# Optimization experiments

Hardware: AMD Instinct MI355X
Metric: run time of the kernel (lower is better)

The kernel has to match this reference:

```python
import jax, jax.numpy as jnp
import numpy as np

B, S, D, H = 2, 2048, 2048, 16
DH = D // H  # 128
ROPE_BASE = 10000.0


def setup_inputs() -> dict:
    key = jax.random.key(0)
    ks = jax.random.split(key, 5)
    scale = 0.02
    return {
        "x": jax.random.normal(ks[0], (B, S, D), dtype=jnp.float32),
        "wq": jax.random.normal(ks[1], (D, D), dtype=jnp.float32) * scale,
        "wk": jax.random.normal(ks[2], (D, D), dtype=jnp.float32) * scale,
        "wv": jax.random.normal(ks[3], (D, D), dtype=jnp.float32) * scale,
        "wo": jax.random.normal(ks[4], (D, D), dtype=jnp.float32) * scale,
    }


def _rope_cache(seq_len, dhead):
    # flash-attn RotaryEmbedding: inv_freq over even dims, full rotary_dim = dhead
    inv_freq = 1.0 / (ROPE_BASE ** (jnp.arange(0, dhead, 2, dtype=jnp.float32) / dhead))
    t = jnp.arange(seq_len, dtype=jnp.float32)
    freqs = jnp.einsum("s,d->sd", t, inv_freq)  # [S, DH/2]
    return jnp.cos(freqs), jnp.sin(freqs)


def _apply_rope_interleaved(t, cos, sin):
    # t: [B, S, H, DH]; interleaved pairs (t[...,0::2], t[...,1::2])
    te, to = t[..., 0::2], t[..., 1::2]
    c = cos[None, :, None, :]
    s = sin[None, :, None, :]
    re = te * c - to * s
    ro = te * s + to * c
    return jnp.stack([re, ro], axis=-1).reshape(t.shape)


def reference(x, wq, wk, wv, wo):
    b, s, d = x.shape
    q = (x @ wq).reshape(b, s, H, DH)
    k = (x @ wk).reshape(b, s, H, DH)
    v = (x @ wv).reshape(b, s, H, DH)

    cos, sin = _rope_cache(s, DH)
    q = _apply_rope_interleaved(q.astype(jnp.float32), cos, sin)
    k = _apply_rope_interleaved(k.astype(jnp.float32), cos, sin)

    # flash_attn_func(causal=True) semantics: bf16 inputs, fp32 softmax, scale 1/sqrt(dhead)
    qb = q.astype(jnp.bfloat16)
    kb = k.astype(jnp.bfloat16)
    vb = v.astype(jnp.bfloat16)
    scale = 1.0 / np.sqrt(DH)
    scores = jnp.einsum("bqhd,bkhd->bhqk", qb, kb,
                        preferred_element_type=jnp.float32) * scale
    causal = jnp.tril(jnp.ones((s, s), dtype=bool))
    scores = jnp.where(causal[None, None], scores, -jnp.inf)
    p = jax.nn.softmax(scores, axis=-1)  # fp32
    attn = jnp.einsum("bhqk,bkhd->bqhd", p.astype(jnp.bfloat16), vb,
                      preferred_element_type=jnp.float32)
    attn = attn.astype(jnp.bfloat16).astype(x.dtype)  # flash returns bf16, then .to(x)
    out = attn.reshape(b, s, d) @ wo
    return out
```

## Files before the change

kernel.cpp:

```cpp
#include <hip/hip_runtime.h>
#include <hip/hip_bf16.h>
#include <stdint.h>

#define B_SZ   2
#define S_LEN  2048
#define DMODEL 2048
#define NH     16
#define DHD    128

typedef __attribute__((ext_vector_type(8))) __bf16 bf16x8;
typedef __attribute__((ext_vector_type(4))) float  f32x4;
typedef __attribute__((ext_vector_type(4))) float  float4v;
typedef __attribute__((ext_vector_type(8))) unsigned short ushort8;
typedef __attribute__((ext_vector_type(4))) unsigned short ushort4v;

__device__ __forceinline__ unsigned short f2bf(float f) {
  unsigned int u = __float_as_uint(f);
  unsigned int r = (u + 0x7fffu + ((u >> 16) & 1u)) >> 16;
  return (unsigned short)r;
}

__device__ __forceinline__ unsigned int cvt_pk_bf16(float lo, float hi) {
  unsigned int r;
  asm("v_cvt_pk_bf16_f32 %0, %1, %2" : "=v"(r) : "v"(lo), "v"(hi));
  return r;
}

__device__ __forceinline__ void async_cp16(void* lds, const void* g) {
  __builtin_amdgcn_global_load_lds(
      (const __attribute__((address_space(1))) void*)g,
      (__attribute__((address_space(3))) void*)lds, 16, 0, 0);
}

__global__ __launch_bounds__(256) void k_cast_bf16(const float* __restrict__ in,
                                                   unsigned short* __restrict__ out,
                                                   int n4) {
  int i = blockIdx.x * 256 + threadIdx.x;
  if (i >= n4) return;
  float4v v = ((const float4v*)in)[i];
  ushort4v o;
  o[0] = f2bf(v[0]); o[1] = f2bf(v[1]); o[2] = f2bf(v[2]); o[3] = f2bf(v[3]);
  ((ushort4v*)out)[i] = o;
}

__global__ __launch_bounds__(256) void k_transpose_all(const float* __restrict__ w0,
                                                       const float* __restrict__ w1,
                                                       const float* __restrict__ w2,
                                                       const float* __restrict__ w3,
                                                       unsigned short* __restrict__ WTbase) {
  __shared__ unsigned short tile[64 * 72];
  const int z = blockIdx.z;
  const float* W = (z == 0) ? w0 : (z == 1) ? w1 : (z == 2) ? w2 : w3;
  unsigned short* WT = WTbase + (size_t)z * 4194304;
  const int n0 = blockIdx.x * 64;
  const int k0 = blockIdx.y * 64;
  const int t = threadIdx.x;
#pragma unroll
  for (int i = 0; i < 4; ++i) {
    int c = t + 256 * i;
    int r = c >> 4, c4 = c & 15;
    float4v v = *(const float4v*)(W + (size_t)(k0 + r) * DMODEL + n0 + c4 * 4);
    ushort4v o;
    o[0] = f2bf(v[0]); o[1] = f2bf(v[1]); o[2] = f2bf(v[2]); o[3] = f2bf(v[3]);
    *(ushort4v*)(&tile[r * 72 + c4 * 4]) = o;
  }
  __syncthreads();
#pragma unroll
  for (int i = 0; i < 2; ++i) {
    int c = t + 256 * i;
    int n = c >> 3, k8 = c & 7;
    ushort8 o;
#pragma unroll
    for (int j = 0; j < 8; ++j) o[j] = tile[(k8 * 8 + j) * 72 + n];
    *(ushort8*)(WT + (size_t)(n0 + n) * DMODEL + k0 + k8 * 8) = o;
  }
}

__global__ __launch_bounds__(256) void k_rope_table(float* __restrict__ cosT,
                                                    float* __restrict__ sinT) {
  int i = blockIdx.x * 256 + threadIdx.x;
  int s = i >> 6, dj = i & 63;
  float e = __expf(-9.210340371976184f * (float)dj * (1.0f / 64.0f));
  float f = (float)s * e;
  cosT[i] = cosf(f);
  sinT[i] = sinf(f);
}

template <int EPI>
__global__ __launch_bounds__(512, 2) void k_gemm128(
    const unsigned short* __restrict__ A,
    const unsigned short* __restrict__ BT,
    float* __restrict__ C0,
    unsigned short* __restrict__ Cq,
    unsigned short* __restrict__ Ck,
    unsigned short* __restrict__ Cv,
    const float* __restrict__ cosT,
    const float* __restrict__ sinT,
    int chn) {
  __shared__ char smem[98304];
  const int tid = threadIdx.x;

  const int xcd = blockIdx.x & 7;
  const int idx = blockIdx.x >> 3;
  const int bm = (xcd >> 2) * 16 + (idx & 15);
  const int bn = (xcd & 3) * chn + (idx >> 4);

  const int gs = (tid & 7) ^ ((tid >> 3) & 7);
  const unsigned short* Abase = A + (size_t)(bm * 128 + (tid >> 3)) * 2048 + gs * 8;
  const unsigned short* Bbase = BT + (size_t)(bn * 256 + (tid >> 3)) * 2048 + gs * 8;
  const int dstA = tid * 16;
  const int dstB = 16384 + tid * 16;

  const int lane = tid & 63, wid = tid >> 6;
  const int wr = wid >> 2, wcn = wid & 3;
  const int lr = lane & 15, hi = lane >> 4;
  int aoff[4][2], boff[4][2];
#pragma unroll
  for (int m = 0; m < 4; ++m) {
    int row = wr * 64 + m * 16 + lr;
#pragma unroll
    for (int k = 0; k < 2; ++k)
      aoff[m][k] = row * 128 + ((((k * 4 + hi)) ^ (row & 7)) << 4);
  }
#pragma unroll
  for (int n = 0; n < 4; ++n) {
    int row = wcn * 64 + n * 16 + lr;
#pragma unroll
    for (int k = 0; k < 2; ++k)
      boff[n][k] = 16384 + row * 128 + ((((k * 4 + hi)) ^ (row & 7)) << 4);
  }

  f32x4 acc[4][4];
#pragma unroll
  for (int m = 0; m < 4; ++m)
#pragma unroll
    for (int n = 0; n < 4; ++n) {
      f32x4 z = {0.f, 0.f, 0.f, 0.f};
      acc[m][n] = z;
    }

#define STG_A(c, t_) do {                                                   \
    const unsigned short* _s = Abase + (t_) * 64;                           \
    async_cp16(smem + (c) * 49152 + dstA, _s);                              \
    async_cp16(smem + (c) * 49152 + dstA + 8192, _s + 64 * 2048);           \
  } while (0)
#define STG_B(c, t_) do {                                                   \
    const unsigned short* _s = Bbase + (t_) * 64;                           \
    async_cp16(smem + (c) * 49152 + dstB, _s);                              \
    async_cp16(smem + (c) * 49152 + dstB + 8192, _s + 64 * 2048);           \
    async_cp16(smem + (c) * 49152 + dstB + 16384, _s + 128 * 2048);         \
    async_cp16(smem + (c) * 49152 + dstB + 24576, _s + 192 * 2048);         \
  } while (0)

  auto tile = [&](int T, int CC, bool DO_A, bool DO_B, int VM) __attribute__((always_inline)) {
    const char* Sb = smem + CC * 49152;
    bf16x8 a0[4], b0[4], a1[4], b1[4];
#pragma unroll
    for (int m = 0; m < 4; ++m) a0[m] = *(const bf16x8*)(Sb + aoff[m][0]);
#pragma unroll
    for (int n = 0; n < 4; ++n) b0[n] = *(const bf16x8*)(Sb + boff[n][0]);
    if (DO_A) STG_A(CC ^ 1, T + 1);
    asm volatile("s_waitcnt lgkmcnt(0)" ::: "memory");
    __builtin_amdgcn_sched_barrier(0);
    __builtin_amdgcn_s_setprio(1);
#pragma unroll
    for (int m = 0; m < 4; ++m) {
      acc[m][0] = __builtin_amdgcn_mfma_f32_16x16x32_bf16(a0[m], b0[0], acc[m][0], 0, 0, 0);
      acc[m][1] = __builtin_amdgcn_mfma_f32_16x16x32_bf16(a0[m], b0[1], acc[m][1], 0, 0, 0);
    }
    __builtin_amdgcn_s_setprio(0);
    __builtin_amdgcn_sched_barrier(0);
#pragma unroll
    for (int m = 0; m < 4; ++m) a1[m] = *(const bf16x8*)(Sb + aoff[m][1]);
#pragma unroll
    for (int n = 0; n < 4; ++n) b1[n] = *(const bf16x8*)(Sb + boff[n][1]);
    __builtin_amdgcn_sched_barrier(0);
    __builtin_amdgcn_s_setprio(1);
#pragma unroll
    for (int m = 0; m < 4; ++m) {
      acc[m][2] = __builtin_amdgcn_mfma_f32_16x16x32_bf16(a0[m], b0[2], acc[m][2], 0, 0, 0);
      acc[m][3] = __builtin_amdgcn_mfma_f32_16x16x32_bf16(a0[m], b0[3], acc[m][3], 0, 0, 0);
    }
    __builtin_amdgcn_s_setprio(0);
    __builtin_amdgcn_s_barrier();
    __builtin_amdgcn_sched_barrier(0);
    asm volatile("s_waitcnt lgkmcnt(0)" ::: "memory");
    __builtin_amdgcn_sched_barrier(0);
    if (DO_B) STG_B(CC, T + 2);
    __builtin_amdgcn_s_setprio(1);
#pragma unroll
    for (int m = 0; m < 4; ++m)
#pragma unroll
      for (int n = 0; n < 4; ++n)
        acc[m][n] = __builtin_amdgcn_mfma_f32_16x16x32_bf16(a1[m], b1[n], acc[m][n], 0, 0, 0);
    __builtin_amdgcn_s_setprio(0);
    if (VM == 0) asm volatile("s_waitcnt vmcnt(4)" ::: "memory");
    else if (VM == 1) asm volatile("s_waitcnt vmcnt(0)" ::: "memory");
    if (VM != 2) {
      __builtin_amdgcn_s_barrier();
      __builtin_amdgcn_sched_barrier(0);
    }
  };

  STG_B(0, 0);
  STG_A(0, 0);
  STG_B(1, 1);
  asm volatile("s_waitcnt vmcnt(4)" ::: "memory");
  __builtin_amdgcn_s_barrier();
  __builtin_amdgcn_sched_barrier(0);

  for (int it = 0; it < 15; ++it) {
    tile(2 * it, 0, true, true, 0);
    tile(2 * it + 1, 1, true, true, 0);
  }
  tile(30, 0, true, false, 1);
  tile(31, 1, false, false, 2);

  const int row_b = bm * 128 + wr * 64 + hi * 4;
  const int col_b = bn * 256 + wcn * 64 + lr;
  if (EPI == 0) {
#pragma unroll
    for (int m = 0; m < 4; ++m)
#pragma unroll
      for (int n = 0; n < 4; ++n) {
        int col = col_b + n * 16;
#pragma unroll
        for (int j = 0; j < 4; ++j) {
          int row = row_b + m * 16 + j;
          C0[(size_t)row * 2048 + col] = acc[m][n][j];
        }
      }
  } else {
    const int sel = bn >> 3;
#pragma unroll
    for (int m = 0; m < 4; ++m) {
#pragma unroll
      for (int n = 0; n < 4; ++n) {
        int col = col_b + n * 16;
        int hh = (col >> 7) & 15, d = col & 127;
        if (sel == 2) {
#pragma unroll
          for (int j = 0; j < 4; ++j) {
            int row = row_b + m * 16 + j;
            int b = row >> 11, s = row & 2047;
            Cv[((size_t)(b * NH + hh) * S_LEN + s) * DHD + d] = f2bf(acc[m][n][j]);
          }
        } else {
          unsigned short* dst = sel ? Ck : Cq;
          int dj = d >> 1;
          float sgn = (d & 1) ? 1.f : -1.f;
#pragma unroll
          for (int j = 0; j < 4; ++j) {
            int row = row_b + m * 16 + j;
            int b = row >> 11, s = row & 2047;
            float v = acc[m][n][j];
            float pp = __shfl_xor(v, 1);
            float cc = cosT[(s << 6) + dj];
            float sn = sinT[(s << 6) + dj];
            dst[((size_t)(b * NH + hh) * S_LEN + s) * DHD + d] = f2bf(v * cc + sgn * pp * sn);
          }
        }
      }
    }
  }
#undef STG_A
#undef STG_B
}

__global__ __launch_bounds__(256) void k_flash_attn(const unsigned short* __restrict__ Qg,
                                                    const unsigned short* __restrict__ Kg,
                                                    const unsigned short* __restrict__ Vg,
                                                    unsigned short* __restrict__ Og) {
  __shared__ unsigned short K_lds[2][64 * 128];
  __shared__ unsigned short VT_lds[2][128 * 64];

  const int pq = blockIdx.x, h = blockIdx.y, b = blockIdx.z;
  const int t = threadIdx.x;
  const int lane = t & 63, wave = t >> 6;
  const int hi = lane >> 4, lr = lane & 15;

  const size_t head = (size_t)(b * NH + h) * (size_t)(S_LEN * DHD);
  const unsigned short* Q = Qg + head;
  const unsigned short* Kp = Kg + head;
  const unsigned short* Vp = Vg + head;

  const int kr0 = t >> 4;
  const int kgc = (t & 15) ^ (kr0 & 7);
  const unsigned short* Kbase = Kp + (size_t)kr0 * DHD + kgc * 8;
  const int kdst = t * 16;

  const int vdc = t & 15, vsp0 = t >> 4;
  const unsigned short* Vbase = Vp + (size_t)(2 * vsp0) * DHD + vdc * 8;
  const int bo0 = 16 * ((vsp0 >> 1) & 3) + 8 * ((vsp0 >> 3) & 1) + 4 * (vsp0 & 1);

  const float sc = 0.08838834764831845f;

  for (int pass = 0; pass < 2; ++pass) {
    const int qt = (pass == 0) ? pq : (15 - pq);
    const int nt = 2 * (qt + 1);
    const int qb0 = qt * 128 + wave * 16;
    const int qb1 = qb0 + 64;

    bf16x8 qf0[4], qf1[4];
    {
      const unsigned short* qr0 = Q + (size_t)(qb0 + lr) * DHD;
      const unsigned short* qr1 = Q + (size_t)(qb1 + lr) * DHD;
#pragma unroll
      for (int kc = 0; kc < 4; ++kc) {
        qf0[kc] = *(const bf16x8*)(qr0 + kc * 32 + hi * 8);
        qf1[kc] = *(const bf16x8*)(qr1 + kc * 32 + hi * 8);
      }
    }

    f32x4 of0[8], of1[8];
#pragma unroll
    for (int i = 0; i < 8; ++i) {
      f32x4 z = {0.f, 0.f, 0.f, 0.f};
      of0[i] = z;
      of1[i] = z;
    }
    float mS0 = -INFINITY, mS1 = -INFINITY;
    float ls0 = 0.f, ls1 = 0.f;

    {
#pragma unroll
      for (int i = 0; i < 4; ++i)
        async_cp16((char*)K_lds[0] + kdst + i * 4096, Kbase + (size_t)(16 * i) * DHD);
      ushort8 va0 = *(const ushort8*)(Vbase);
      ushort8 vb0 = *(const ushort8*)(Vbase + DHD);
      ushort8 va1 = *(const ushort8*)(Vbase + (size_t)32 * DHD);
      ushort8 vb1 = *(const ushort8*)(Vbase + (size_t)33 * DHD);
#pragma unroll
      for (int j = 0; j < 8; ++j) {
        int row = vdc * 8 + j;
        int swz = ((j ^ vdc) & 7) << 4;
        *(unsigned int*)((char*)VT_lds[0] + row * 128 + (bo0 ^ swz)) =
            (unsigned int)va0[j] | ((unsigned int)vb0[j] << 16);
        *(unsigned int*)((char*)VT_lds[0] + row * 128 + ((bo0 | 64) ^ swz)) =
            (unsigned int)va1[j] | ((unsigned int)vb1[j] << 16);
      }
    }
    __syncthreads();

    for (int tt = 0; tt < nt; ++tt) {
      const int cur = tt & 1;
      const int kv0 = tt * 64;
      const bool more = (tt + 1 < nt);

      ushort8 va0, vb0, va1, vb1;
      if (more) {
        const unsigned short* ks = Kbase + (size_t)(kv0 + 64) * DHD;
#pragma unroll
        for (int i = 0; i < 4; ++i)
          async_cp16((char*)K_lds[cur ^ 1] + kdst + i * 4096, ks + (size_t)(16 * i) * DHD);
        const unsigned short* vs = Vbase + (size_t)(kv0 + 64) * DHD;
        va0 = *(const ushort8*)(vs);
        vb0 = *(const ushort8*)(vs + DHD);
        va1 = *(const ushort8*)(vs + (size_t)32 * DHD);
        vb1 = *(const ushort8*)(vs + (size_t)33 * DHD);
      }

      const char* Kb = (const char*)K_lds[cur];
      f32x4 sf0[4], sf1[4];
#pragma unroll
      for (int n = 0; n < 4; ++n) {
        f32x4 z = {0.f, 0.f, 0.f, 0.f};
        sf0[n] = z;
        sf1[n] = z;
      }
      __builtin_amdgcn_s_setprio(1);
#pragma unroll
      for (int n = 0; n < 4; ++n) {
        const int kr = n * 16 + lr;
        const int kswz = (kr & 7) << 4;
#pragma unroll
        for (int kc = 0; kc < 4; ++kc) {
          bf16x8 kf = *(const bf16x8*)(Kb + kr * 256 + ((kc * 64 + hi * 16) ^ kswz));
          sf0[n] = __builtin_amdgcn_mfma_f32_16x16x32_bf16(kf, qf0[kc], sf0[n], 0, 0, 0);
          sf1[n] = __builtin_amdgcn_mfma_f32_16x16x32_bf16(kf, qf1[kc], sf1[n], 0, 0, 0);
        }
      }
      __builtin_amdgcn_s_setprio(0);

      unsigned int pk0[4][2], pk1[4][2];
      float cb0[4], cb1[4];
      const bool act0 = kv0 <= qb0 + 15;
      const bool act1 = kv0 <= qb1 + 15;

#define SOFTMAX_SET(SF, MS, LS, PK, CB, QB, ACT) do {                        \
    if (ACT) {                                                               \
      float p_[4][4];                                                        \
      float mx = -INFINITY;                                                  \
      const int qrow_ = (QB) + lr;                                           \
      if (kv0 + 63 > (QB)) {                                                 \
        _Pragma("unroll")                                                    \
        for (int n = 0; n < 4; ++n)                                          \
          _Pragma("unroll")                                                  \
          for (int j = 0; j < 4; ++j) {                                      \
            int kvcol = kv0 + n * 16 + hi * 4 + j;                           \
            float v = (kvcol > qrow_) ? -INFINITY : SF[n][j];                \
            p_[n][j] = v;                                                    \
            mx = fmaxf(mx, v);                                               \
          }                                                                  \
      } else {                                                               \
        _Pragma("unroll")                                                    \
        for (int n = 0; n < 4; ++n)                                          \
          _Pragma("unroll")                                                  \
          for (int j = 0; j < 4; ++j) {                                      \
            float v = SF[n][j];                                              \
            p_[n][j] = v;                                                    \
            mx = fmaxf(mx, v);                                               \
          }                                                                  \
      }                                                                      \
      mx = fmaxf(mx, __shfl_xor(mx, 16));                                    \
      mx = fmaxf(mx, __shfl_xor(mx, 32));                                    \
      float mn = fmaxf(MS, mx);                                              \
      float corr = __expf((MS - mn) * sc);                                   \
      MS = mn;                                                               \
      float mns = mn * sc;                                                   \
      float rs = 0.f;                                                        \
      _Pragma("unroll")                                                      \
      for (int n = 0; n < 4; ++n)                                            \
        _Pragma("unroll")                                                    \
        for (int j = 0; j < 4; ++j) {                                        \
          float e = __expf(__builtin_fmaf(p_[n][j], sc, -mns));              \
          p_[n][j] = e;                                                      \
          rs += e;                                                           \
        }                                                                    \
      rs += __shfl_xor(rs, 16);                                              \
      rs += __shfl_xor(rs, 32);                                              \
      LS = LS * corr + rs;                                                   \
      _Pragma("unroll")                                                      \
      for (int n = 0; n < 4; ++n) {                                          \
        PK[n][0] = cvt_pk_bf16(p_[n][0], p_[n][1]);                          \
        PK[n][1] = cvt_pk_bf16(p_[n][2], p_[n][3]);                          \
      }                                                                      \
      _Pragma("unroll")                                                      \
      for (int j = 0; j < 4; ++j) CB[j] = __shfl(corr, hi * 4 + j);          \
    } else {                                                                 \
      _Pragma("unroll")                                                      \
      for (int n = 0; n < 4; ++n) { PK[n][0] = 0u; PK[n][1] = 0u; }          \
      _Pragma("unroll")                                                      \
      for (int j = 0; j < 4; ++j) CB[j] = 1.f;                               \
    }                                                                        \
  } while (0)

      SOFTMAX_SET(sf0, mS0, ls0, pk0, cb0, qb0, act0);
      SOFTMAX_SET(sf1, mS1, ls1, pk1, cb1, qb1, act1);
#undef SOFTMAX_SET

#pragma unroll
      for (int nd = 0; nd < 8; ++nd)
#pragma unroll
        for (int j = 0; j < 4; ++j) {
          of0[nd][j] *= cb0[j];
          of1[nd][j] *= cb1[j];
        }

      const char* Vb = (const char*)VT_lds[cur];
      __builtin_amdgcn_s_setprio(1);
#pragma unroll
      for (int kc = 0; kc < 2; ++kc) {
        union { unsigned int u[4]; bf16x8 v; } pa0, pa1;
        pa0.u[0] = pk0[2 * kc][0];     pa0.u[1] = pk0[2 * kc][1];
        pa0.u[2] = pk0[2 * kc + 1][0]; pa0.u[3] = pk0[2 * kc + 1][1];
        pa1.u[0] = pk1[2 * kc][0];     pa1.u[1] = pk1[2 * kc][1];
        pa1.u[2] = pk1[2 * kc + 1][0]; pa1.u[3] = pk1[2 * kc + 1][1];
#pragma unroll
        for (int nd = 0; nd < 8; ++nd) {
          const int vr = nd * 16 + lr;
          const int vswz = ((vr & 7) ^ ((vr >> 3) & 7)) << 4;
          bf16x8 vf = *(const bf16x8*)(Vb + vr * 128 + ((kc * 64 + hi * 16) ^ vswz));
          of0[nd] = __builtin_amdgcn_mfma_f32_16x16x32_bf16(pa0.v, vf, of0[nd], 0, 0, 0);
          of1[nd] = __builtin_amdgcn_mfma_f32_16x16x32_bf16(pa1.v, vf, of1[nd], 0, 0, 0);
        }
      }
      __builtin_amdgcn_s_setprio(0);

      if (more) {
        char* Vw = (char*)VT_lds[cur ^ 1];
#pragma unroll
        for (int j = 0; j < 8; ++j) {
          int row = vdc * 8 + j;
          int swz = ((j ^ vdc) & 7) << 4;
          *(unsigned int*)(Vw + row * 128 + (bo0 ^ swz)) =
              (unsigned int)va0[j] | ((unsigned int)vb0[j] << 16);
          *(unsigned int*)(Vw + row * 128 + ((bo0 | 64) ^ swz)) =
              (unsigned int)va1[j] | ((unsigned int)vb1[j] << 16);
        }
      }
      __syncthreads();
    }

    float inv0[4], inv1[4];
#pragma unroll
    for (int j = 0; j < 4; ++j) {
      inv0[j] = 1.0f / __shfl(ls0, hi * 4 + j);
      inv1[j] = 1.0f / __shfl(ls1, hi * 4 + j);
    }
#pragma unroll
    for (int nd = 0; nd < 8; ++nd)
#pragma unroll
      for (int j = 0; j < 4; ++j) {
        int qr0 = qb0 + hi * 4 + j;
        int qr1 = qb1 + hi * 4 + j;
        Og[((size_t)(b * S_LEN + qr0) * NH + h) * DHD + nd * 16 + lr] = f2bf(of0[nd][j] * inv0[j]);
        Og[((size_t)(b * S_LEN + qr1) * NH + h) * DHD + nd * 16 + lr] = f2bf(of1[nd][j] * inv1[j]);
      }
  }
}

extern "C" void kernel_launch(void* const* d_in, const int* in_sizes, int n_in,
                              void* d_out, int out_size, void* d_ws, size_t ws_size,
                              hipStream_t stream) {
  const float* x  = (const float*)d_in[0];
  const float* wq = (const float*)d_in[1];
  const float* wk = (const float*)d_in[2];
  const float* wv = (const float*)d_in[3];
  const float* wo = (const float*)d_in[4];
  float* out = (float*)d_out;

  char* ws = (char*)d_ws;
  unsigned short* xb    = (unsigned short*)(ws);
  unsigned short* wqT   = (unsigned short*)(ws + 16777216);
  unsigned short* woT   = (unsigned short*)(ws + 41943040);
  unsigned short* qb    = (unsigned short*)(ws + 50331648);
  unsigned short* kb    = (unsigned short*)(ws + 67108864);
  unsigned short* vb    = (unsigned short*)(ws + 83886080);
  float*          cosT  = (float*)(ws + 100663296);
  float*          sinT  = (float*)(ws + 101187584);
  unsigned short* attnb = xb;

  k_cast_bf16<<<8192, 256, 0, stream>>>(x, xb, 2097152);
  dim3 tg(32, 32, 4);
  k_transpose_all<<<tg, 256, 0, stream>>>(wq, wk, wv, wo, wqT);
  k_rope_table<<<512, 256, 0, stream>>>(cosT, sinT);

  k_gemm128<1><<<768, 512, 0, stream>>>(xb, wqT, nullptr, qb, kb, vb, cosT, sinT, 6);

  dim3 ga(8, 16, 2);
  k_flash_attn<<<ga, 256, 0, stream>>>(qb, kb, vb, attnb);

  k_gemm128<0><<<256, 512, 0, stream>>>(attnb, woT, out, nullptr, nullptr, nullptr,
                                        nullptr, nullptr, 2);
}
```

Measured before the change: 258.1 us.

## Fuse prep kernels into one launch and split flash-attn into per-tile XCD-aware blocks

Merges the x cast, the four weight transposes and the rope table into one kernel that branches on block index, removing two launches. Flash attention moves from 256 blocks that each handle a paired light and heavy query tile to 512 blocks of one tile each. The new ordering issues heavy tiles first and groups each (batch, head) onto one XCD so that XCD's L2 can reuse its K/V. This gives more parallelism and longest-first scheduling, but drops the explicit load balancing of the paired passes.

```diff
diff --git a/kernel.cpp b/kernel.cpp
--- a/kernel.cpp
+++ b/kernel.cpp
@@ -32,58 +32,58 @@
       (__attribute__((address_space(3))) void*)lds, 16, 0, 0);
 }
 
-__global__ __launch_bounds__(256) void k_cast_bf16(const float* __restrict__ in,
-                                                   unsigned short* __restrict__ out,
-                                                   int n4) {
-  int i = blockIdx.x * 256 + threadIdx.x;
-  if (i >= n4) return;
-  float4v v = ((const float4v*)in)[i];
-  ushort4v o;
-  o[0] = f2bf(v[0]); o[1] = f2bf(v[1]); o[2] = f2bf(v[2]); o[3] = f2bf(v[3]);
-  ((ushort4v*)out)[i] = o;
-}
-
-__global__ __launch_bounds__(256) void k_transpose_all(const float* __restrict__ w0,
-                                                       const float* __restrict__ w1,
-                                                       const float* __restrict__ w2,
-                                                       const float* __restrict__ w3,
-                                                       unsigned short* __restrict__ WTbase) {
+__global__ __launch_bounds__(256) void k_prep_all(const float* __restrict__ x,
+                                                  const float* __restrict__ w0,
+                                                  const float* __restrict__ w1,
+                                                  const float* __restrict__ w2,
+                                                  const float* __restrict__ w3,
+                                                  unsigned short* __restrict__ xb,
+                                                  unsigned short* __restrict__ WTbase,
+                                                  float* __restrict__ cosT,
+                                                  float* __restrict__ sinT) {
   __shared__ unsigned short tile[64 * 72];
-  const int z = blockIdx.z;
-  const float* W = (z == 0) ? w0 : (z == 1) ? w1 : (z == 2) ? w2 : w3;
-  unsigned short* WT = WTbase + (size_t)z * 4194304;
-  const int n0 = blockIdx.x * 64;
-  const int k0 = blockIdx.y * 64;
+  const int bx = blockIdx.x;
   const int t = threadIdx.x;
-#pragma unroll
-  for (int i = 0; i < 4; ++i) {
-    int c = t + 256 * i;
-    int r = c >> 4, c4 = c & 15;
-    float4v v = *(const float4v*)(W + (size_t)(k0 + r) * DMODEL + n0 + c4 * 4);
+  if (bx < 4096) {
+    const int z = bx >> 10;
+    const int wi = bx & 1023;
+    const float* W = (z == 0) ? w0 : (z == 1) ? w1 : (z == 2) ? w2 : w3;
+    unsigned short* WT = WTbase + (size_t)z * 4194304;
+    const int n0 = (wi & 31) * 64;
+    const int k0 = (wi >> 5) * 64;
+#pragma unroll
+    for (int i = 0; i < 4; ++i) {
+      int c = t + 256 * i;
+      int r = c >> 4, c4 = c & 15;
+      float4v v = *(const float4v*)(W + (size_t)(k0 + r) * DMODEL + n0 + c4 * 4);
+      ushort4v o;
+      o[0] = f2bf(v[0]); o[1] = f2bf(v[1]); o[2] = f2bf(v[2]); o[3] = f2bf(v[3]);
+      *(ushort4v*)(&tile[r * 72 + c4 * 4]) = o;
+    }
+    __syncthreads();
+#pragma unroll
+    for (int i = 0; i < 2; ++i) {
+      int c = t + 256 * i;
+      int n = c >> 3, k8 = c & 7;
+      ushort8 o;
+#pragma unroll
+      for (int j = 0; j < 8; ++j) o[j] = tile[(k8 * 8 + j) * 72 + n];
+      *(ushort8*)(WT + (size_t)(n0 + n) * DMODEL + k0 + k8 * 8) = o;
+    }
+  } else if (bx < 12288) {
+    int i = (bx - 4096) * 256 + t;
+    float4v v = ((const float4v*)x)[i];
     ushort4v o;
     o[0] = f2bf(v[0]); o[1] = f2bf(v[1]); o[2] = f2bf(v[2]); o[3] = f2bf(v[3]);
-    *(ushort4v*)(&tile[r * 72 + c4 * 4]) = o;
-  }
-  __syncthreads();
-#pragma unroll
-  for (int i = 0; i < 2; ++i) {
-    int c = t + 256 * i;
-    int n = c >> 3, k8 = c & 7;
-    ushort8 o;
-#pragma unroll
-    for (int j = 0; j < 8; ++j) o[j] = tile[(k8 * 8 + j) * 72 + n];
-    *(ushort8*)(WT + (size_t)(n0 + n) * DMODEL + k0 + k8 * 8) = o;
-  }
-}
-
-__global__ __launch_bounds__(256) void k_rope_table(float* __restrict__ cosT,
-                                                    float* __restrict__ sinT) {
-  int i = blockIdx.x * 256 + threadIdx.x;
-  int s = i >> 6, dj = i & 63;
-  float e = __expf(-9.210340371976184f * (float)dj * (1.0f / 64.0f));
-  float f = (float)s * e;
-  cosT[i] = cosf(f);
-  sinT[i] = sinf(f);
+    ((ushort4v*)xb)[i] = o;
+  } else {
+    int i = (bx - 12288) * 256 + t;
+    int s = i >> 6, dj = i & 63;
+    float e = __expf(-9.210340371976184f * (float)dj * (1.0f / 64.0f));
+    float f = (float)s * e;
+    cosT[i] = cosf(f);
+    sinT[i] = sinf(f);
+  }
 }
 
 template <int EPI>
@@ -274,7 +274,13 @@
   __shared__ unsigned short K_lds[2][64 * 128];
   __shared__ unsigned short VT_lds[2][128 * 64];
 
-  const int pq = blockIdx.x, h = blockIdx.y, b = blockIdx.z;
+  const int bx = blockIdx.x;
+  const int xcd = bx & 7;
+  const int u = bx >> 3;
+  const int hb = xcd + 8 * (u & 3);
+  const int h = hb & 15, b = hb >> 4;
+  const int qt = (u < 32) ? (8 + (u >> 2)) : (7 - ((u - 32) >> 2));
+
   const int t = threadIdx.x;
   const int lane = t & 63, wave = t >> 6;
   const int hi = lane >> 4, lr = lane & 15;
@@ -295,97 +301,95 @@
 
   const float sc = 0.08838834764831845f;
 
-  for (int pass = 0; pass < 2; ++pass) {
-    const int qt = (pass == 0) ? pq : (15 - pq);
-    const int nt = 2 * (qt + 1);
-    const int qb0 = qt * 128 + wave * 16;
-    const int qb1 = qb0 + 64;
-
-    bf16x8 qf0[4], qf1[4];
-    {
-      const unsigned short* qr0 = Q + (size_t)(qb0 + lr) * DHD;
-      const unsigned short* qr1 = Q + (size_t)(qb1 + lr) * DHD;
+  const int nt = 2 * (qt + 1);
+  const int qb0 = qt * 128 + wave * 16;
+  const int qb1 = qb0 + 64;
+
+  bf16x8 qf0[4], qf1[4];
+  {
+    const unsigned short* qr0 = Q + (size_t)(qb0 + lr) * DHD;
+    const unsigned short* qr1 = Q + (size_t)(qb1 + lr) * DHD;
+#pragma unroll
+    for (int kc = 0; kc < 4; ++kc) {
+      qf0[kc] = *(const bf16x8*)(qr0 + kc * 32 + hi * 8);
+      qf1[kc] = *(const bf16x8*)(qr1 + kc * 32 + hi * 8);
+    }
+  }
+
+  f32x4 of0[8], of1[8];
+#pragma unroll
+  for (int i = 0; i < 8; ++i) {
+    f32x4 z = {0.f, 0.f, 0.f, 0.f};
+    of0[i] = z;
+    of1[i] = z;
+  }
+  float mS0 = -INFINITY, mS1 = -INFINITY;
+  float ls0 = 0.f, ls1 = 0.f;
+
+  {
+#pragma unroll
+    for (int i = 0; i < 4; ++i)
+      async_cp16((char*)K_lds[0] + kdst + i * 4096, Kbase + (size_t)(16 * i) * DHD);
+    ushort8 va0 = *(const ushort8*)(Vbase);
+    ushort8 vb0 = *(const ushort8*)(Vbase + DHD);
+    ushort8 va1 = *(const ushort8*)(Vbase + (size_t)32 * DHD);
+    ushort8 vb1 = *(const ushort8*)(Vbase + (size_t)33 * DHD);
+#pragma unroll
+    for (int j = 0; j < 8; ++j) {
+      int row = vdc * 8 + j;
+      int swz = ((j ^ vdc) & 7) << 4;
+      *(unsigned int*)((char*)VT_lds[0] + row * 128 + (bo0 ^ swz)) =
+          (unsigned int)va0[j] | ((unsigned int)vb0[j] << 16);
+      *(unsigned int*)((char*)VT_lds[0] + row * 128 + ((bo0 | 64) ^ swz)) =
+          (unsigned int)va1[j] | ((unsigned int)vb1[j] << 16);
+    }
+  }
+  __syncthreads();
+
+  for (int tt = 0; tt < nt; ++tt) {
+    const int cur = tt & 1;
+    const int kv0 = tt * 64;
+    const bool more = (tt + 1 < nt);
+
+    ushort8 va0, vb0, va1, vb1;
+    if (more) {
+      const unsigned short* ks = Kbase + (size_t)(kv0 + 64) * DHD;
+#pragma unroll
+      for (int i = 0; i < 4; ++i)
+        async_cp16((char*)K_lds[cur ^ 1] + kdst + i * 4096, ks + (size_t)(16 * i) * DHD);
+      const unsigned short* vs = Vbase + (size_t)(kv0 + 64) * DHD;
+      va0 = *(const ushort8*)(vs);
+      vb0 = *(const ushort8*)(vs + DHD);
+      va1 = *(const ushort8*)(vs + (size_t)32 * DHD);
+      vb1 = *(const ushort8*)(vs + (size_t)33 * DHD);
+    }
+
+    const char* Kb = (const char*)K_lds[cur];
+    f32x4 sf0[4], sf1[4];
+#pragma unroll
+    for (int n = 0; n < 4; ++n) {
+      f32x4 z = {0.f, 0.f, 0.f, 0.f};
+      sf0[n] = z;
+      sf1[n] = z;
+    }
+    __builtin_amdgcn_s_setprio(1);
+#pragma unroll
+    for (int n = 0; n < 4; ++n) {
+      const int kr = n * 16 + lr;
+      const int kswz = (kr & 7) << 4;
 #pragma unroll
       for (int kc = 0; kc < 4; ++kc) {
-        qf0[kc] = *(const bf16x8*)(qr0 + kc * 32 + hi * 8);
-        qf1[kc] = *(const bf16x8*)(qr1 + kc * 32 + hi * 8);
+        bf16x8 kf = *(const bf16x8*)(Kb + kr * 256 + ((kc * 64 + hi * 16) ^ kswz));
+        sf0[n] = __builtin_amdgcn_mfma_f32_16x16x32_bf16(kf, qf0[kc], sf0[n], 0, 0, 0);
+        sf1[n] = __builtin_amdgcn_mfma_f32_16x16x32_bf16(kf, qf1[kc], sf1[n], 0, 0, 0);
       }
     }
-
-    f32x4 of0[8], of1[8];
-#pragma unroll
-    for (int i = 0; i < 8; ++i) {
-      f32x4 z = {0.f, 0.f, 0.f, 0.f};
-      of0[i] = z;
-      of1[i] = z;
-    }
-    float mS0 = -INFINITY, mS1 = -INFINITY;
-    float ls0 = 0.f, ls1 = 0.f;
-
-    {
-#pragma unroll
-      for (int i = 0; i < 4; ++i)
-        async_cp16((char*)K_lds[0] + kdst + i * 4096, Kbase + (size_t)(16 * i) * DHD);
-      ushort8 va0 = *(const ushort8*)(Vbase);
-      ushort8 vb0 = *(const ushort8*)(Vbase + DHD);
-      ushort8 va1 = *(const ushort8*)(Vbase + (size_t)32 * DHD);
-      ushort8 vb1 = *(const ushort8*)(Vbase + (size_t)33 * DHD);
-#pragma unroll
-      for (int j = 0; j < 8; ++j) {
-        int row = vdc * 8 + j;
-        int swz = ((j ^ vdc) & 7) << 4;
-        *(unsigned int*)((char*)VT_lds[0] + row * 128 + (bo0 ^ swz)) =
-            (unsigned int)va0[j] | ((unsigned int)vb0[j] << 16);
-        *(unsigned int*)((char*)VT_lds[0] + row * 128 + ((bo0 | 64) ^ swz)) =
-            (unsigned int)va1[j] | ((unsigned int)vb1[j] << 16);
-      }
-    }
-    __syncthreads();
-
-    for (int tt = 0; tt < nt; ++tt) {
-      const int cur = tt & 1;
-      const int kv0 = tt * 64;
-      const bool more = (tt + 1 < nt);
-
-      ushort8 va0, vb0, va1, vb1;
-      if (more) {
-        const unsigned short* ks = Kbase + (size_t)(kv0 + 64) * DHD;
-#pragma unroll
-        for (int i = 0; i < 4; ++i)
-          async_cp16((char*)K_lds[cur ^ 1] + kdst + i * 4096, ks + (size_t)(16 * i) * DHD);
-        const unsigned short* vs = Vbase + (size_t)(kv0 + 64) * DHD;
-        va0 = *(const ushort8*)(vs);
-        vb0 = *(const ushort8*)(vs + DHD);
-        va1 = *(const ushort8*)(vs + (size_t)32 * DHD);
-        vb1 = *(const ushort8*)(vs + (size_t)33 * DHD);
-      }
-
-      const char* Kb = (const char*)K_lds[cur];
-      f32x4 sf0[4], sf1[4];
-#pragma unroll
-      for (int n = 0; n < 4; ++n) {
-        f32x4 z = {0.f, 0.f, 0.f, 0.f};
-        sf0[n] = z;
-        sf1[n] = z;
-      }
-      __builtin_amdgcn_s_setprio(1);
-#pragma unroll
-      for (int n = 0; n < 4; ++n) {
-        const int kr = n * 16 + lr;
-        const int kswz = (kr & 7) << 4;
-#pragma unroll
-        for (int kc = 0; kc < 4; ++kc) {
-          bf16x8 kf = *(const bf16x8*)(Kb + kr * 256 + ((kc * 64 + hi * 16) ^ kswz));
-          sf0[n] = __builtin_amdgcn_mfma_f32_16x16x32_bf16(kf, qf0[kc], sf0[n], 0, 0, 0);
-          sf1[n] = __builtin_amdgcn_mfma_f32_16x16x32_bf16(kf, qf1[kc], sf1[n], 0, 0, 0);
-        }
-      }
-      __builtin_amdgcn_s_setprio(0);
-
-      unsigned int pk0[4][2], pk1[4][2];
-      float cb0[4], cb1[4];
-      const bool act0 = kv0 <= qb0 + 15;
-      const bool act1 = kv0 <= qb1 + 15;
+    __builtin_amdgcn_s_setprio(0);
+
+    unsigned int pk0[4][2], pk1[4][2];
+    float cb0[4], cb1[4];
+    const bool act0 = kv0 <= qb0 + 15;
+    const bool act1 = kv0 <= qb1 + 15;
 
 #define SOFTMAX_SET(SF, MS, LS, PK, CB, QB, ACT) do {                        \
     if (ACT) {                                                               \
@@ -445,69 +449,68 @@
     }                                                                        \
   } while (0)
 
-      SOFTMAX_SET(sf0, mS0, ls0, pk0, cb0, qb0, act0);
-      SOFTMAX_SET(sf1, mS1, ls1, pk1, cb1, qb1, act1);
+    SOFTMAX_SET(sf0, mS0, ls0, pk0, cb0, qb0, act0);
+    SOFTMAX_SET(sf1, mS1, ls1, pk1, cb1, qb1, act1);
 #undef SOFTMAX_SET
 
 #pragma unroll
-      for (int nd = 0; nd < 8; ++nd)
-#pragma unroll
-        for (int j = 0; j < 4; ++j) {
-          of0[nd][j] *= cb0[j];
-          of1[nd][j] *= cb1[j];
-        }
-
-      const char* Vb = (const char*)VT_lds[cur];
-      __builtin_amdgcn_s_setprio(1);
-#pragma unroll
-      for (int kc = 0; kc < 2; ++kc) {
-        union { unsigned int u[4]; bf16x8 v; } pa0, pa1;
-        pa0.u[0] = pk0[2 * kc][0];     pa0.u[1] = pk0[2 * kc][1];
-        pa0.u[2] = pk0[2 * kc + 1][0]; pa0.u[3] = pk0[2 * kc + 1][1];
-        pa1.u[0] = pk1[2 * kc][0];     pa1.u[1] = pk1[2 * kc][1];
-        pa1.u[2] = pk1[2 * kc + 1][0]; pa1.u[3] = pk1[2 * kc + 1][1];
-#pragma unroll
-        for (int nd = 0; nd < 8; ++nd) {
-          const int vr = nd * 16 + lr;
-          const int vswz = ((vr & 7) ^ ((vr >> 3) & 7)) << 4;
-          bf16x8 vf = *(const bf16x8*)(Vb + vr * 128 + ((kc * 64 + hi * 16) ^ vswz));
-          of0[nd] = __builtin_amdgcn_mfma_f32_16x16x32_bf16(pa0.v, vf, of0[nd], 0, 0, 0);
-          of1[nd] = __builtin_amdgcn_mfma_f32_16x16x32_bf16(pa1.v, vf, of1[nd], 0, 0, 0);
-        }
+    for (int nd = 0; nd < 8; ++nd)
+#pragma unroll
+      for (int j = 0; j < 4; ++j) {
+        of0[nd][j] *= cb0[j];
+        of1[nd][j] *= cb1[j];
       }
-      __builtin_amdgcn_s_setprio(0);
-
-      if (more) {
-        char* Vw = (char*)VT_lds[cur ^ 1];
-#pragma unroll
-        for (int j = 0; j < 8; ++j) {
-          int row = vdc * 8 + j;
-          int swz = ((j ^ vdc) & 7) << 4;
-          *(unsigned int*)(Vw + row * 128 + (bo0 ^ swz)) =
-              (unsigned int)va0[j] | ((unsigned int)vb0[j] << 16);
-          *(unsigned int*)(Vw + row * 128 + ((bo0 | 64) ^ swz)) =
-              (unsigned int)va1[j] | ((unsigned int)vb1[j] << 16);
-        }
+
+    const char* Vb = (const char*)VT_lds[cur];
+    __builtin_amdgcn_s_setprio(1);
+#pragma unroll
+    for (int kc = 0; kc < 2; ++kc) {
+      union { unsigned int u[4]; bf16x8 v; } pa0, pa1;
+      pa0.u[0] = pk0[2 * kc][0];     pa0.u[1] = pk0[2 * kc][1];
+      pa0.u[2] = pk0[2 * kc + 1][0]; pa0.u[3] = pk0[2 * kc + 1][1];
+      pa1.u[0] = pk1[2 * kc][0];     pa1.u[1] = pk1[2 * kc][1];
+      pa1.u[2] = pk1[2 * kc + 1][0]; pa1.u[3] = pk1[2 * kc + 1][1];
+#pragma unroll
+      for (int nd = 0; nd < 8; ++nd) {
+        const int vr = nd * 16 + lr;
+        const int vswz = ((vr & 7) ^ ((vr >> 3) & 7)) << 4;
+        bf16x8 vf = *(const bf16x8*)(Vb + vr * 128 + ((kc * 64 + hi * 16) ^ vswz));
+        of0[nd] = __builtin_amdgcn_mfma_f32_16x16x32_bf16(pa0.v, vf, of0[nd], 0, 0, 0);
+        of1[nd] = __builtin_amdgcn_mfma_f32_16x16x32_bf16(pa1.v, vf, of1[nd], 0, 0, 0);
       }
-      __syncthreads();
-    }
-
-    float inv0[4], inv1[4];
+    }
+    __builtin_amdgcn_s_setprio(0);
+
+    if (more) {
+      char* Vw = (char*)VT_lds[cur ^ 1];
+#pragma unroll
+      for (int j = 0; j < 8; ++j) {
+        int row = vdc * 8 + j;
+        int swz = ((j ^ vdc) & 7) << 4;
+        *(unsigned int*)(Vw + row * 128 + (bo0 ^ swz)) =
+            (unsigned int)va0[j] | ((unsigned int)vb0[j] << 16);
+        *(unsigned int*)(Vw + row * 128 + ((bo0 | 64) ^ swz)) =
+            (unsigned int)va1[j] | ((unsigned int)vb1[j] << 16);
+      }
+    }
+    __syncthreads();
+  }
+
+  float inv0[4], inv1[4];
+#pragma unroll
+  for (int j = 0; j < 4; ++j) {
+    inv0[j] = 1.0f / __shfl(ls0, hi * 4 + j);
+    inv1[j] = 1.0f / __shfl(ls1, hi * 4 + j);
+  }
+#pragma unroll
+  for (int nd = 0; nd < 8; ++nd)
 #pragma unroll
     for (int j = 0; j < 4; ++j) {
-      inv0[j] = 1.0f / __shfl(ls0, hi * 4 + j);
-      inv1[j] = 1.0f / __shfl(ls1, hi * 4 + j);
-    }
-#pragma unroll
-    for (int nd = 0; nd < 8; ++nd)
-#pragma unroll
-      for (int j = 0; j < 4; ++j) {
-        int qr0 = qb0 + hi * 4 + j;
-        int qr1 = qb1 + hi * 4 + j;
-        Og[((size_t)(b * S_LEN + qr0) * NH + h) * DHD + nd * 16 + lr] = f2bf(of0[nd][j] * inv0[j]);
-        Og[((size_t)(b * S_LEN + qr1) * NH + h) * DHD + nd * 16 + lr] = f2bf(of1[nd][j] * inv1[j]);
-      }
-  }
+      int qr0 = qb0 + hi * 4 + j;
+      int qr1 = qb1 + hi * 4 + j;
+      Og[((size_t)(b * S_LEN + qr0) * NH + h) * DHD + nd * 16 + lr] = f2bf(of0[nd][j] * inv0[j]);
+      Og[((size_t)(b * S_LEN + qr1) * NH + h) * DHD + nd * 16 + lr] = f2bf(of1[nd][j] * inv1[j]);
+    }
 }
 
 extern "C" void kernel_launch(void* const* d_in, const int* in_sizes, int n_in,
@@ -531,15 +534,11 @@
   float*          sinT  = (float*)(ws + 101187584);
   unsigned short* attnb = xb;
 
-  k_cast_bf16<<<8192, 256, 0, stream>>>(x, xb, 2097152);
-  dim3 tg(32, 32, 4);
-  k_transpose_all<<<tg, 256, 0, stream>>>(wq, wk, wv, wo, wqT);
-  k_rope_table<<<512, 256, 0, stream>>>(cosT, sinT);
+  k_prep_all<<<12800, 256, 0, stream>>>(x, wq, wk, wv, wo, xb, wqT, cosT, sinT);
 
   k_gemm128<1><<<768, 512, 0, stream>>>(xb, wqT, nullptr, qb, kb, vb, cosT, sinT, 6);
 
-  dim3 ga(8, 16, 2);
-  k_flash_attn<<<ga, 256, 0, stream>>>(qb, kb, vb, attnb);
+  k_flash_attn<<<512, 256, 0, stream>>>(qb, kb, vb, attnb);
 
   k_gemm128<0><<<256, 512, 0, stream>>>(attnb, woT, out, nullptr, nullptr, nullptr,
                                         nullptr, nullptr, 2);
```

Result: faster. 250.5 us (-2.9%).
